# Kernel tuning notes

Hardware: AMD Instinct MI355X
Metric: run time of the kernel (lower is better)

Reference implementation:

```python
import jax, jax.numpy as jnp
import numpy as np

B, S, H, D = 4, 2048, 12, 64
HID = H * D  # 768
EPS = 1e-5


def _layer_norm(h, w, b):
    mu = jnp.mean(h, axis=-1, keepdims=True)
    var = jnp.mean((h - mu) ** 2, axis=-1, keepdims=True)
    return w * (h - mu) / jnp.sqrt(var + EPS) + b


def setup_inputs() -> dict:
    key = jax.random.key(0)
    ks = jax.random.split(key, 12)
    sc = 1.0 / np.sqrt(HID)
    inp = {
        "x": jax.random.normal(ks[0], (B, S, HID), jnp.float32),
        "ln1_w": jnp.ones((HID,), jnp.float32),
        "ln1_b": jnp.zeros((HID,), jnp.float32),
        "Wq": jax.random.normal(ks[1], (HID, HID), jnp.float32) * sc,
        "bq": jnp.zeros((HID,), jnp.float32),
        "Wk": jax.random.normal(ks[2], (HID, HID), jnp.float32) * sc,
        "bk": jnp.zeros((HID,), jnp.float32),
        "Wv": jax.random.normal(ks[3], (HID, HID), jnp.float32) * sc,
        "bv": jnp.zeros((HID,), jnp.float32),
        "Wo": jax.random.normal(ks[4], (HID, HID), jnp.float32) * sc,
        "bo": jnp.zeros((HID,), jnp.float32),
        "ln2_w": jnp.ones((HID,), jnp.float32),
        "ln2_b": jnp.zeros((HID,), jnp.float32),
        "W1": jax.random.normal(ks[5], (HID, 4 * HID), jnp.float32) * sc,
        "b1": jnp.zeros((4 * HID,), jnp.float32),
        "W2": jax.random.normal(ks[6], (4 * HID, HID), jnp.float32) * (1.0 / np.sqrt(4 * HID)),
        "b2": jnp.zeros((HID,), jnp.float32),
    }
    return inp


def _split_heads(t):
    # (B, S, H*D) -> (B, H, S, D)
    b, s, _ = t.shape
    return t.reshape(b, s, H, -1).transpose(0, 2, 1, 3)


def _merge_heads(t):
    # (B, H, S, D) -> (B, S, H*D)
    b, h, s, d = t.shape
    return t.transpose(0, 2, 1, 3).reshape(b, s, h * d)


def _attention(h, Wq, bq, Wk, bk, Wv, bv, Wo, bo):
    q = _split_heads(h @ Wq + bq)  # (B,H,S,D)
    k = _split_heads(h @ Wk + bk)
    v = _split_heads(h @ Wv + bv)
    scores = jnp.einsum("bhqd,bhkd->bhqk", q, k) / jnp.sqrt(jnp.asarray(D, h.dtype))
    causal = jnp.tril(jnp.ones((q.shape[2], q.shape[2]), bool))  # (S,S)
    scores = jnp.where(causal, scores, jnp.finfo(scores.dtype).min)
    w = jax.nn.softmax(scores, axis=-1)
    out = jnp.einsum("bhqk,bhkd->bhqd", w, v)
    return _merge_heads(out) @ Wo + bo


def reference(x, ln1_w, ln1_b, Wq, bq, Wk, bk, Wv, bv, Wo, bo, ln2_w, ln2_b, W1, b1, W2, b2):
    # Pre-LN transformer block: x + attn(LN(x)); then x + MLP(LN(x))
    a = _attention(_layer_norm(x, ln1_w, ln1_b), Wq, bq, Wk, bk, Wv, bv, Wo, bo)
    x = x + a
    h = _layer_norm(x, ln2_w, ln2_b)
    m = jax.nn.gelu(h @ W1 + b1, approximate=False) @ W2 + b2
    return x + m
```

## Files before the change

kernel.cpp:

```cpp
#include <hip/hip_runtime.h>
#include <cmath>
#include <stdint.h>

typedef unsigned short u16;
typedef __attribute__((ext_vector_type(8))) short short8;
typedef __attribute__((ext_vector_type(4))) float f32x4;
typedef __attribute__((ext_vector_type(4))) unsigned int u32x4;

#define HID 768
#define FF  3072
#define SEQ 2048
#define NHEAD 12
#define NROWS 8192

__device__ __forceinline__ float bf2f(u16 u){ return __uint_as_float(((unsigned)u)<<16); }
__device__ __forceinline__ u16 f2bf(float f){
  unsigned x = __float_as_uint(f);
  x += 0x7fffu + ((x>>16)&1u);
  return (u16)(x>>16);
}
__device__ __forceinline__ unsigned cvtpk(float a, float b){
  unsigned r;
  asm("v_cvt_pk_bf16_f32 %0, %1, %2" : "=v"(r) : "v"(a), "v"(b));
  return r;
}
__device__ __forceinline__ void gload16(const void* g, void* l){
  __builtin_amdgcn_global_load_lds((const __attribute__((address_space(1))) unsigned*)g,
                                   (__attribute__((address_space(3))) unsigned*)l, 16, 0, 0);
}

__global__ __launch_bounds__(256) void wconv(const float* __restrict__ in,
                                             u16* __restrict__ out, int K, int N)
{
  __shared__ float t[32][33];
  const int bk = blockIdx.x*32, bn = blockIdx.y*32;
  const int tn = threadIdx.x & 31, tk = threadIdx.x >> 5;
  #pragma unroll
  for (int j=0;j<4;++j)
    t[tk+8*j][tn] = in[(size_t)(bk+tk+8*j)*N + bn + tn];
  __syncthreads();
  #pragma unroll
  for (int j=0;j<4;++j)
    out[(size_t)(bn+tk+8*j)*K + bk + tn] = f2bf(t[tn][tk+8*j]);
}

__global__ __launch_bounds__(256) void tconv(const u16* __restrict__ in,
                                             u16* __restrict__ out, int K, int N)
{
  __shared__ u16 t[32][34];
  const int bk = blockIdx.x*32, bn = blockIdx.y*32;
  const int tn = threadIdx.x & 31, tk = threadIdx.x >> 5;
  #pragma unroll
  for (int j=0;j<4;++j)
    t[tk+8*j][tn] = in[(size_t)(bk+tk+8*j)*N + bn + tn];
  __syncthreads();
  #pragma unroll
  for (int j=0;j<4;++j)
    out[(size_t)(bn+tk+8*j)*K + bk + tn] = t[tn][tk+8*j];
}

__global__ __launch_bounds__(256) void ln_k(const float* __restrict__ in,
    const float* __restrict__ gw, const float* __restrict__ gb,
    u16* __restrict__ out)
{
  const int row = blockIdx.x*4 + (threadIdx.x>>6);
  const int l = threadIdx.x & 63;
  const float* p = in + (size_t)row*HID;
  float4 v[3];
  float s=0.f, ss=0.f;
  #pragma unroll
  for (int j=0;j<3;++j){
    v[j] = *(const float4*)(p + j*256 + l*4);
    s  += v[j].x + v[j].y + v[j].z + v[j].w;
    ss += v[j].x*v[j].x + v[j].y*v[j].y + v[j].z*v[j].z + v[j].w*v[j].w;
  }
  #pragma unroll
  for (int m=1;m<64;m<<=1){
    s  += __shfl_xor(s,  m, 64);
    ss += __shfl_xor(ss, m, 64);
  }
  const float mu = s * (1.f/768.f);
  const float rstd = rsqrtf(ss*(1.f/768.f) - mu*mu + 1e-5f);
  #pragma unroll
  for (int j=0;j<3;++j){
    const float4 wv = *(const float4*)(gw + j*256 + l*4);
    const float4 bv = *(const float4*)(gb + j*256 + l*4);
    ushort4 o;
    o.x = f2bf((v[j].x-mu)*rstd*wv.x + bv.x);
    o.y = f2bf((v[j].y-mu)*rstd*wv.y + bv.y);
    o.z = f2bf((v[j].z-mu)*rstd*wv.z + bv.z);
    o.w = f2bf((v[j].w-mu)*rstd*wv.w + bv.w);
    *(ushort4*)(out + (size_t)row*HID + j*256 + l*4) = o;
  }
}

template<int MODE>
__global__ __launch_bounds__(256) void gemm_bt(const u16* __restrict__ A,
    const u16* __restrict__ Bt, const float* __restrict__ bias0,
    const float* __restrict__ bias1, const float* __restrict__ bias2,
    const float* __restrict__ res, void* __restrict__ outp,
    int N, int K, long wstride, long ostride)
{
  __shared__ __align__(16) u16 sA[3][128*32];
  __shared__ __align__(16) u16 sB[3][128*32];
  const int tid = threadIdx.x, l = tid&63, w = tid>>6;
  const int wr = w>>1, wc = w&1, hi = l>>4, lo = l&15;
  const int bm = blockIdx.x*128, bn = blockIdx.y*128;
  const int z = blockIdx.z;
  const u16* Bz = Bt + (size_t)z * (size_t)wstride;
  const float* bias = (z==0) ? bias0 : ((z==1)? bias1 : bias2);

  const u16* Arow = A  + (size_t)bm*K;
  const u16* Brow = Bz + (size_t)bn*K;

  const f32x4 zv = {0.f,0.f,0.f,0.f};
  f32x4 acc[4][4];
  #pragma unroll
  for (int i=0;i<4;++i)
    #pragma unroll
    for (int j=0;j<4;++j) acc[i][j] = zv;

  const int r0_ = tid>>2, off_ = (tid&3)*8;
  const int r1_ = r0_ + 64;

  #define STAGE(T, BUF) do { \
    const int kt_ = (T) << 5; \
    gload16(Arow + (size_t)r0_*K + kt_ + off_, (char*)sA[BUF] + tid*16); \
    gload16(Arow + (size_t)r1_*K + kt_ + off_, (char*)sA[BUF] + (tid+256)*16); \
    gload16(Brow + (size_t)r0_*K + kt_ + off_, (char*)sB[BUF] + tid*16); \
    gload16(Brow + (size_t)r1_*K + kt_ + off_, (char*)sB[BUF] + (tid+256)*16); \
  } while(0)

  const int NT = K >> 5;
  STAGE(0, 0);
  STAGE(1, 1);
  asm volatile("s_waitcnt vmcnt(4)" ::: "memory");
  __builtin_amdgcn_s_barrier();
  __builtin_amdgcn_sched_barrier(0);

  int cur = 0;
  for (int t=0; t<NT; ++t){
    int nb = cur+2; if (nb>=3) nb-=3;
    if (t+2 < NT) STAGE(t+2, nb);
    short8 af[4], bfv[4];
    #pragma unroll
    for (int i=0;i<4;++i){
      af[i]  = *(const short8*)(sA[cur] + (wr*64 + i*16 + lo)*32 + hi*8);
      bfv[i] = *(const short8*)(sB[cur] + (wc*64 + i*16 + lo)*32 + hi*8);
    }
    #pragma unroll
    for (int mi=0;mi<4;++mi)
      #pragma unroll
      for (int ni=0;ni<4;++ni)
        acc[mi][ni] = __builtin_amdgcn_mfma_f32_16x16x32_bf16(af[mi], bfv[ni], acc[mi][ni], 0,0,0);
    if (t+1 < NT){
      if (t+2 < NT) asm volatile("s_waitcnt vmcnt(4)" ::: "memory");
      else          asm volatile("s_waitcnt vmcnt(0)" ::: "memory");
      __builtin_amdgcn_s_barrier();
      __builtin_amdgcn_sched_barrier(0);
    }
    cur = (cur+1==3) ? 0 : cur+1;
  }
  #undef STAGE

  #pragma unroll
  for (int mi=0;mi<4;++mi)
    #pragma unroll
    for (int ni=0;ni<4;++ni){
      const int r0 = bm + wr*64 + mi*16 + 4*hi;
      const int cc = bn + wc*64 + ni*16 + lo;
      const float bv = bias[cc];
      #pragma unroll
      for (int g=0; g<4; ++g){
        const size_t idx = (size_t)(r0+g)*N + cc;
        float v = acc[mi][ni][g] + bv;
        if (MODE == 0){
          ((u16*)outp + (size_t)z*(size_t)ostride)[idx] = f2bf(v);
        } else if (MODE == 1){
          ((float*)outp)[idx] = res[idx] + v;
        } else {
          float u = v*(0.7978845608f + 0.0356774081f*v*v);
          float e = __expf(2.f*u);
          float th = 1.f - 2.f/(1.f + e);
          ((u16*)outp)[idx] = f2bf(0.5f*v*(1.f + th));
        }
      }
    }
}

__global__ __launch_bounds__(256, 4) void attn_k(const u16* __restrict__ Qm,
                                                 const u16* __restrict__ Km,
                                                 const u16* __restrict__ Vt,
                                                 u16* __restrict__ Om)
{
  __shared__ __align__(16) u16 sK [64*64];
  __shared__ __align__(16) u16 sVT[64*64];
  const int tid = threadIdx.x, l = tid & 63, w = tid >> 6;
  const int hi = l >> 4, lo = l & 15;
  const int idx = blockIdx.x;
  const int qb = 31 - (idx / 48);
  const int bh = idx % 48;
  const int b = bh / NHEAD, h = bh - (bh / NHEAD) * NHEAD;
  const size_t rb = (size_t)b * SEQ;
  const int qw = qb*64 + w*16;

  short8 qf[2];
  #pragma unroll
  for (int ks=0; ks<2; ++ks){
    short8 t = *(const short8*)(Qm + (rb + qw + lo)*HID + h*64 + ks*32 + hi*8);
    #pragma unroll
    for (int i=0;i<8;++i) t[i] = (short)f2bf(bf2f((u16)t[i]) * 0.1803368801f);
    qf[ks] = t;
  }

  const f32x4 zv = {0.f,0.f,0.f,0.f};
  f32x4 oa[4] = {zv, zv, zv, zv};
  float m = -INFINITY, lsum = 0.f;
  const int srcA = (((2*hi)  & 3) << 4) | lo;
  const int srcB = (((2*hi+1)& 3) << 4) | lo;

  for (int t=0; t<=qb; ++t){
    const int kv0 = t*64;
    __syncthreads();
    #pragma unroll
    for (int j=0;j<2;++j){
      int c = tid + 256*j;
      int row = c >> 3;
      int d0 = ((c&7) ^ (row&7))*8;
      gload16(Km + (rb + kv0 + row)*HID + h*64 + d0, (char*)sK + c*16);
    }
    #pragma unroll
    for (int j=0;j<2;++j){
      int c = tid + 256*j;
      int row = c >> 3;
      int k0 = ((c&7) ^ (row&7))*8;
      gload16(Vt + (size_t)(h*64 + row)*NROWS + rb + kv0 + k0, (char*)sVT + c*16);
    }
    __syncthreads();

    f32x4 sc[4] = {zv, zv, zv, zv};
    #pragma unroll
    for (int ks=0;ks<2;++ks){
      #pragma unroll
      for (int ni=0;ni<4;++ni){
        short8 kf = *(const short8*)(sK + (ni*16 + lo)*64 + ((ks*32 + hi*8) ^ ((lo&7)*8)));
        sc[ni] = __builtin_amdgcn_mfma_f32_16x16x32_bf16(kf, qf[ks], sc[ni], 0,0,0);
      }
    }

    if (t == qb){
      #pragma unroll
      for (int ni=0;ni<4;++ni)
        #pragma unroll
        for (int g=0; g<4; ++g){
          int kg = kv0 + ni*16 + 4*hi + g;
          if (kg > qw + lo) sc[ni][g] = -INFINITY;
        }
    }

    float a0 = fmaxf(fmaxf(sc[0][0], sc[0][1]), fmaxf(sc[0][2], sc[0][3]));
    float a1 = fmaxf(fmaxf(sc[1][0], sc[1][1]), fmaxf(sc[1][2], sc[1][3]));
    float a2 = fmaxf(fmaxf(sc[2][0], sc[2][1]), fmaxf(sc[2][2], sc[2][3]));
    float a3 = fmaxf(fmaxf(sc[3][0], sc[3][1]), fmaxf(sc[3][2], sc[3][3]));
    float pm = fmaxf(fmaxf(a0, a1), fmaxf(a2, a3));
    pm = fmaxf(pm, __shfl_xor(pm, 16, 64));
    pm = fmaxf(pm, __shfl_xor(pm, 32, 64));

    if (!__all(pm - m <= 10.f)){
      const float mnew = fmaxf(m, pm);
      const float alpha = __builtin_amdgcn_exp2f(m - mnew);
      lsum *= alpha;
      #pragma unroll
      for (int nd=0;nd<4;++nd){
        oa[nd][0]*=alpha; oa[nd][1]*=alpha; oa[nd][2]*=alpha; oa[nd][3]*=alpha;
      }
      m = mnew;
    }

    float ps = 0.f;
    #pragma unroll
    for (int ni=0;ni<4;++ni)
      #pragma unroll
      for (int g=0; g<4; ++g){
        float e = __builtin_amdgcn_exp2f(sc[ni][g] - m);
        sc[ni][g] = e;
        ps += e;
      }
    ps += __shfl_xor(ps, 16, 64);
    ps += __shfl_xor(ps, 32, 64);
    lsum += ps;

    #pragma unroll
    for (int ks=0;ks<2;++ks){
      unsigned pkA0 = cvtpk(sc[2*ks  ][0], sc[2*ks  ][1]);
      unsigned pkA1 = cvtpk(sc[2*ks  ][2], sc[2*ks  ][3]);
      unsigned pkB0 = cvtpk(sc[2*ks+1][0], sc[2*ks+1][1]);
      unsigned pkB1 = cvtpk(sc[2*ks+1][2], sc[2*ks+1][3]);
      unsigned a0u = (unsigned)__shfl((int)pkA0, srcA, 64);
      unsigned b0u = (unsigned)__shfl((int)pkB0, srcA, 64);
      unsigned a1u = (unsigned)__shfl((int)pkA1, srcA, 64);
      unsigned b1u = (unsigned)__shfl((int)pkB1, srcA, 64);
      unsigned a2u = (unsigned)__shfl((int)pkA0, srcB, 64);
      unsigned b2u = (unsigned)__shfl((int)pkB0, srcB, 64);
      unsigned a3u = (unsigned)__shfl((int)pkA1, srcB, 64);
      unsigned b3u = (unsigned)__shfl((int)pkB1, srcB, 64);
      union { u32x4 u; short8 s; } pf;
      pf.u = (u32x4){ (hi<2)?a0u:b0u, (hi<2)?a1u:b1u, (hi<2)?a2u:b2u, (hi<2)?a3u:b3u };

      #pragma unroll
      for (int nd=0;nd<4;++nd){
        short8 vf = *(const short8*)(sVT + (nd*16 + lo)*64 + ((ks*32 + hi*8) ^ ((lo&7)*8)));
        oa[nd] = __builtin_amdgcn_mfma_f32_16x16x32_bf16(vf, pf.s, oa[nd], 0,0,0);
      }
    }
  }

  const float inv = 1.f / lsum;
  #pragma unroll
  for (int nd=0;nd<4;++nd){
    ushort4 o;
    o.x = f2bf(oa[nd][0]*inv);
    o.y = f2bf(oa[nd][1]*inv);
    o.z = f2bf(oa[nd][2]*inv);
    o.w = f2bf(oa[nd][3]*inv);
    *(ushort4*)(Om + (rb + qw + lo)*HID + h*64 + nd*16 + 4*hi) = o;
  }
}

extern "C" void kernel_launch(void* const* d_in, const int* in_sizes, int n_in,
                              void* d_out, int out_size, void* d_ws, size_t ws_size,
                              hipStream_t stream)
{
  const float* x    = (const float*)d_in[0];
  const float* ln1w = (const float*)d_in[1];
  const float* ln1b = (const float*)d_in[2];
  const float* Wq   = (const float*)d_in[3];
  const float* bq   = (const float*)d_in[4];
  const float* Wk   = (const float*)d_in[5];
  const float* bk   = (const float*)d_in[6];
  const float* Wv   = (const float*)d_in[7];
  const float* bv   = (const float*)d_in[8];
  const float* Wo   = (const float*)d_in[9];
  const float* bo   = (const float*)d_in[10];
  const float* ln2w = (const float*)d_in[11];
  const float* ln2b = (const float*)d_in[12];
  const float* W1   = (const float*)d_in[13];
  const float* b1   = (const float*)d_in[14];
  const float* W2   = (const float*)d_in[15];
  const float* b2   = (const float*)d_in[16];

  u16* wq_t = (u16*)d_ws;
  u16* wk_t = wq_t + 589824;
  u16* wv_t = wk_t + 589824;
  u16* wo_t = wv_t + 589824;
  u16* w1_t = wo_t + 589824;
  u16* w2_t = w1_t + 2359296;
  u16* hbf  = w2_t + 2359296;
  u16* qb_  = hbf + 6291456;
  u16* kb_  = qb_ + 6291456;
  u16* vb_  = kb_ + 6291456;
  u16* atb  = vb_ + 6291456;
  u16* ub   = qb_;
  float* x2 = (float*)(atb + 6291456);

  const size_t need = 102236160ull;
  if (ws_size < need) return;

  dim3 blk(256);
  wconv<<<dim3(24,24), blk, 0, stream>>>(Wq, wq_t, 768, 768);
  wconv<<<dim3(24,24), blk, 0, stream>>>(Wk, wk_t, 768, 768);
  wconv<<<dim3(24,24), blk, 0, stream>>>(Wv, wv_t, 768, 768);
  wconv<<<dim3(24,24), blk, 0, stream>>>(Wo, wo_t, 768, 768);
  wconv<<<dim3(24,96), blk, 0, stream>>>(W1, w1_t, 768, 3072);
  wconv<<<dim3(96,24), blk, 0, stream>>>(W2, w2_t, 3072, 768);

  ln_k<<<2048, blk, 0, stream>>>(x, ln1w, ln1b, hbf);

  gemm_bt<0><<<dim3(64,6,3), blk, 0, stream>>>(hbf, wq_t, bq, bk, bv,
      nullptr, (void*)qb_, 768, 768, 589824L, 6291456L);
  tconv<<<dim3(256,24), blk, 0, stream>>>(vb_, hbf, 8192, 768);

  attn_k<<<dim3(1536), blk, 0, stream>>>(qb_, kb_, hbf, atb);

  gemm_bt<1><<<dim3(64,6,1), blk, 0, stream>>>(atb, wo_t, bo, bo, bo,
      x, (void*)x2, 768, 768, 0L, 0L);

  ln_k<<<2048, blk, 0, stream>>>(x2, ln2w, ln2b, hbf);

  gemm_bt<2><<<dim3(64,24,1), blk, 0, stream>>>(hbf, w1_t, b1, b1, b1,
      nullptr, (void*)ub, 3072, 768, 0L, 0L);

  gemm_bt<1><<<dim3(64,6,1), blk, 0, stream>>>(ub, w2_t, b2, b2, b2,
      x2, d_out, 768, 3072, 0L, 0L);
}
```

Baseline: 404.7 us.

## Switch GEMM LDS pipeline from triple to double buffering

Shrinks the shared-memory staging in the bf16 GEMM from three buffers to two and prefetches only one k-tile ahead. The explicit vmcnt waits and sched barriers are replaced by plain __syncthreads. This halves the prefetch depth while cutting LDS use, which may let more blocks fit per CU. The cost is less latency hiding and a full wait on outstanding loads at every iteration's barrier.

```diff
diff --git a/kernel.cpp b/kernel.cpp
--- a/kernel.cpp
+++ b/kernel.cpp
@@ -101,8 +101,8 @@
     const float* __restrict__ res, void* __restrict__ outp,
     int N, int K, long wstride, long ostride)
 {
-  __shared__ __align__(16) u16 sA[3][128*32];
-  __shared__ __align__(16) u16 sB[3][128*32];
+  __shared__ __align__(16) u16 sA[2][128*32];
+  __shared__ __align__(16) u16 sB[2][128*32];
   const int tid = threadIdx.x, l = tid&63, w = tid>>6;
   const int wr = w>>1, wc = w&1, hi = l>>4, lo = l&15;
   const int bm = blockIdx.x*128, bn = blockIdx.y*128;
@@ -123,25 +123,22 @@
   const int r0_ = tid>>2, off_ = (tid&3)*8;
   const int r1_ = r0_ + 64;
 
-  #define STAGE(T, BUF) do { \
-    const int kt_ = (T) << 5; \
-    gload16(Arow + (size_t)r0_*K + kt_ + off_, (char*)sA[BUF] + tid*16); \
-    gload16(Arow + (size_t)r1_*K + kt_ + off_, (char*)sA[BUF] + (tid+256)*16); \
-    gload16(Brow + (size_t)r0_*K + kt_ + off_, (char*)sB[BUF] + tid*16); \
-    gload16(Brow + (size_t)r1_*K + kt_ + off_, (char*)sB[BUF] + (tid+256)*16); \
-  } while(0)
+  gload16(Arow + (size_t)r0_*K + off_, (char*)sA[0] + tid*16);
+  gload16(Arow + (size_t)r1_*K + off_, (char*)sA[0] + (tid+256)*16);
+  gload16(Brow + (size_t)r0_*K + off_, (char*)sB[0] + tid*16);
+  gload16(Brow + (size_t)r1_*K + off_, (char*)sB[0] + (tid+256)*16);
+  __syncthreads();
 
   const int NT = K >> 5;
-  STAGE(0, 0);
-  STAGE(1, 1);
-  asm volatile("s_waitcnt vmcnt(4)" ::: "memory");
-  __builtin_amdgcn_s_barrier();
-  __builtin_amdgcn_sched_barrier(0);
-
   int cur = 0;
   for (int t=0; t<NT; ++t){
-    int nb = cur+2; if (nb>=3) nb-=3;
-    if (t+2 < NT) STAGE(t+2, nb);
+    if (t+1 < NT){
+      const int kt = (t+1) << 5;
+      gload16(Arow + (size_t)r0_*K + kt + off_, (char*)sA[cur^1] + tid*16);
+      gload16(Arow + (size_t)r1_*K + kt + off_, (char*)sA[cur^1] + (tid+256)*16);
+      gload16(Brow + (size_t)r0_*K + kt + off_, (char*)sB[cur^1] + tid*16);
+      gload16(Brow + (size_t)r1_*K + kt + off_, (char*)sB[cur^1] + (tid+256)*16);
+    }
     short8 af[4], bfv[4];
     #pragma unroll
     for (int i=0;i<4;++i){
@@ -153,15 +150,9 @@
       #pragma unroll
       for (int ni=0;ni<4;++ni)
         acc[mi][ni] = __builtin_amdgcn_mfma_f32_16x16x32_bf16(af[mi], bfv[ni], acc[mi][ni], 0,0,0);
-    if (t+1 < NT){
-      if (t+2 < NT) asm volatile("s_waitcnt vmcnt(4)" ::: "memory");
-      else          asm volatile("s_waitcnt vmcnt(0)" ::: "memory");
-      __builtin_amdgcn_s_barrier();
-      __builtin_amdgcn_sched_barrier(0);
-    }
-    cur = (cur+1==3) ? 0 : cur+1;
-  }
-  #undef STAGE
+    __syncthreads();
+    cur ^= 1;
+  }
 
   #pragma unroll
   for (int mi=0;mi<4;++mi)
```

Result: faster. 380.4 us (-6.0%).
